# Optimization experiments

Measured on AMD Instinct MI355X. Metric: run time of the kernel, lower is better.

Reference implementation:

```python
import jax, jax.numpy as jnp
import numpy as np

N_RAYS = 4096
WORLD_LEN = 160
K0_DIM = 12
WIDTH = 128
VIEWPE = 4
BG_LEN = 0.2
XYZ_MIN = -1.0 - BG_LEN
XYZ_MAX = 1.0 + BG_LEN
ALPHA_INIT = 1e-4
ACT_SHIFT = float(np.log(1.0 / (1.0 - ALPHA_INIT) - 1.0))  # density bias shift
BG = 1.0  # background color (render_kwargs['bg'])
DIM0 = 3 + 3 * VIEWPE * 2 + K0_DIM  # 39


def grid_interp(grid, pts):
    """Trilinear interpolation (align_corners=True). grid: [C,R,R,R], pts: [M,3] world coords -> [M,C]."""
    R = grid.shape[1]
    g = (pts - XYZ_MIN) / (XYZ_MAX - XYZ_MIN) * (R - 1)
    g = jnp.clip(g, 0.0, R - 1)
    g0 = jnp.clip(jnp.floor(g).astype(jnp.int32), 0, R - 2)
    f = g - g0
    x0, y0, z0 = g0[:, 0], g0[:, 1], g0[:, 2]
    fx, fy, fz = f[:, 0], f[:, 1], f[:, 2]

    def gat(i, j, k):
        return grid[:, i, j, k]  # [C, M]

    c00 = gat(x0, y0, z0) * (1 - fz) + gat(x0, y0, z0 + 1) * fz
    c01 = gat(x0, y0 + 1, z0) * (1 - fz) + gat(x0, y0 + 1, z0 + 1) * fz
    c10 = gat(x0 + 1, y0, z0) * (1 - fz) + gat(x0 + 1, y0, z0 + 1) * fz
    c11 = gat(x0 + 1, y0 + 1, z0) * (1 - fz) + gat(x0 + 1, y0 + 1, z0 + 1) * fz
    c0 = c00 * (1 - fy) + c01 * fy
    c1 = c10 * (1 - fy) + c11 * fy
    return (c0 * (1 - fx) + c1 * fx).T  # [M, C]


def setup_inputs() -> dict:
    key = jax.random.key(0)
    ks = jax.random.split(key, 11)
    return {
        "rays_o": jax.random.normal(ks[0], (N_RAYS, 3), jnp.float32) * 0.3,
        "rays_d": jax.random.normal(ks[1], (N_RAYS, 3), jnp.float32),
        "viewdirs": jax.random.normal(ks[2], (N_RAYS, 3), jnp.float32),
        "density_grid": jax.random.normal(ks[3], (1, WORLD_LEN, WORLD_LEN, WORLD_LEN), jnp.float32),
        "k0_grid": jax.random.normal(ks[4], (K0_DIM, WORLD_LEN, WORLD_LEN, WORLD_LEN), jnp.float32),
        "w0": jax.random.normal(ks[5], (DIM0, WIDTH), jnp.float32) * 0.05,
        "b0": jnp.zeros((WIDTH,), jnp.float32),
        "w1": jax.random.normal(ks[6], (WIDTH, WIDTH), jnp.float32) * 0.05,
        "b1": jnp.zeros((WIDTH,), jnp.float32),
        "w2": jax.random.normal(ks[7], (WIDTH, 3), jnp.float32) * 0.05,
        "b2": jnp.zeros((3,), jnp.float32),
        "stepsize": 1,
    }


def reference(rays_o, rays_d, viewdirs, density_grid, k0_grid, w0, b0, w1, b1, w2, b2, stepsize):
    sqrt3 = float(np.sqrt(3.0))
    # --- sample_ray: sample points along rays in the contracted domain ---
    N_inner = int(2.0 / (2.0 + 2.0 * BG_LEN) * sqrt3 * WORLD_LEN / stepsize) + 1
    N_outer = int(N_inner * max(0.01, BG_LEN / 2.0))
    b_inner = jnp.linspace(0.0, 2.0 * sqrt3, N_inner + 1)
    b_outer = 2.0 * sqrt3 / jnp.linspace(1.0, 0.001, N_outer + 1)
    t = jnp.concatenate([(b_inner[1:] + b_inner[:-1]) * 0.5,
                         (b_outer[1:] + b_outer[:-1]) * 0.5])  # [P]
    # scene_center = 0, scene_radius = 1 for xyz_min=-1, xyz_max=1
    rd = rays_d / jnp.linalg.norm(rays_d, axis=-1, keepdims=True)
    pts = rays_o[:, None, :] + rd[:, None, :] * t[None, :, None]  # [N,P,3]
    norm = jnp.max(jnp.abs(pts), axis=-1, keepdims=True)
    safe = jnp.maximum(norm, 1e-9)
    pts = jnp.where(norm <= 1.0, pts, pts / safe * (1.0 + BG_LEN - BG_LEN / safe))
    N, P = pts.shape[0], pts.shape[1]
    flat = pts.reshape(-1, 3)  # [M,3]

    # --- density -> alpha (Raw2Alpha); mask_cache is all-True, fast_color_thres=0 ---
    interval = float(stepsize) * 1.0  # voxel_size_ratio == 1
    dens = grid_interp(density_grid, flat)[:, 0].reshape(N, P)
    alpha = 1.0 - jnp.power(1.0 + jnp.exp(dens + ACT_SHIFT), -interval)

    # --- Alphas2Weights: per-ray alpha compositing ---
    T = jnp.cumprod(1.0 - alpha, axis=1)
    T_excl = jnp.concatenate([jnp.ones((N, 1), T.dtype), T[:, :-1]], axis=1)
    weights = alpha * T_excl  # [N,P]
    alphainv_last = T[:, -1]  # [N]

    # --- k0 features + view-dependent MLP ---
    k0 = grid_interp(k0_grid, flat).reshape(N, P, K0_DIM)
    vf = (2.0 ** jnp.arange(VIEWPE)).astype(rays_o.dtype)
    ve = (viewdirs[..., None] * vf).reshape(N, -1)
    vemb = jnp.concatenate([viewdirs, jnp.sin(ve), jnp.cos(ve)], axis=-1)  # [N, 3+24]
    feat = jnp.concatenate(
        [k0, jnp.broadcast_to(vemb[:, None, :], (N, P, vemb.shape[-1]))], axis=-1)  # [N,P,39]
    h = jax.nn.relu(feat @ w0 + b0)
    h = jax.nn.relu(h @ w1 + b1)
    rgb = jax.nn.sigmoid(h @ w2 + b2)  # [N,P,3]

    # --- volume rendering ---
    rgb_marched = jnp.sum(weights[..., None] * rgb, axis=1) + alphainv_last[:, None] * BG
    return rgb_marched  # [N,3]
```

## Files before the change

### kernel.cpp

```cpp
#include <hip/hip_runtime.h>

#define NRAYS 4096
#define PSAMP 254
#define NIN   231
#define GR    160
#define GR2   25600
#define GR3   4096000
#define SROW  136

typedef __attribute__((ext_vector_type(8))) short bf16x8;
typedef __attribute__((ext_vector_type(4))) float f32x4;

__device__ __forceinline__ unsigned short f2bf(float x) {
    union { float f; unsigned u; } v; v.f = x;
    return (unsigned short)((v.u + 0x7fffu + ((v.u >> 16) & 1u)) >> 16);
}
__device__ __forceinline__ float sigmoidf_(float x) { return 1.0f / (1.0f + __expf(-x)); }

__device__ __forceinline__ unsigned packh2(float a, float b) {
    union { _Float16 h; unsigned short u; } ua, ub;
    ua.h = (_Float16)a; ub.h = (_Float16)b;
    return (unsigned)ua.u | ((unsigned)ub.u << 16);
}
__device__ __forceinline__ float h2f(unsigned u16) {
    union { unsigned short u; _Float16 h; } v; v.u = (unsigned short)u16;
    return (float)v.h;
}
__device__ __forceinline__ float cget(const uint4& q, int c) {
    const unsigned w = ((const unsigned*)&q)[c >> 1];
    return h2f((c & 1) ? (w >> 16) : (w & 0xffffu));
}

__global__ void prepack(const float* __restrict__ w, unsigned short* __restrict__ out,
                        int K, int N, int ldw, int NT, int KS) {
    const int idx = blockIdx.x * 256 + threadIdx.x;
    if (idx >= NT * KS * 64) return;
    const int l  = idx & 63, f = idx >> 6;
    const int ks = f % KS,  nt = f / KS;
    const int n  = nt * 16 + (l & 15);
    const int k0 = ks * 32 + (l >> 4) * 8;
    unsigned p[4];
    #pragma unroll
    for (int q = 0; q < 4; q++) {
        const int ka = k0 + 2 * q, kb = ka + 1;
        const float va = (ka < K && n < N) ? w[ka * ldw + n] : 0.0f;
        const float vb = (kb < K && n < N) ? w[kb * ldw + n] : 0.0f;
        p[q] = (unsigned)f2bf(va) | ((unsigned)f2bf(vb) << 16);
    }
    uint4 v; v.x = p[0]; v.y = p[1]; v.z = p[2]; v.w = p[3];
    ((uint4*)out)[idx] = v;
}

__global__ __launch_bounds__(256) void repack_grid(
    const float* __restrict__ dg, const float* __restrict__ k0g,
    unsigned short* __restrict__ pg)
{
    const int i2 = blockIdx.x * 256 + threadIdx.x;
    if (i2 >= GR3 / 2) return;
    unsigned ow[16];
    #pragma unroll
    for (int c = 0; c < 12; c += 2) {
        const float2 va = ((const float2*)(k0g + (size_t)c       * GR3))[i2];
        const float2 vb = ((const float2*)(k0g + (size_t)(c + 1) * GR3))[i2];
        ow[(c >> 1)]     = packh2(va.x, vb.x);
        ow[8 + (c >> 1)] = packh2(va.y, vb.y);
    }
    const float2 dv = ((const float2*)dg)[i2];
    ow[6]  = packh2(dv.x, 0.0f);
    ow[14] = packh2(dv.y, 0.0f);
    ow[7] = 0u; ow[15] = 0u;
    uint4* dst = (uint4*)(pg + (size_t)i2 * 32);
    dst[0] = make_uint4(ow[0],  ow[1],  ow[2],  ow[3]);
    dst[1] = make_uint4(ow[4],  ow[5],  ow[6],  ow[7]);
    dst[2] = make_uint4(ow[8],  ow[9],  ow[10], ow[11]);
    dst[3] = make_uint4(ow[12], ow[13], ow[14], ow[15]);
}

__global__ __launch_bounds__(256, 2) void voxgo_mfma_pk(
    const float* __restrict__ rays_o, const float* __restrict__ rays_d,
    const float* __restrict__ viewdirs,
    const unsigned short* __restrict__ pg,
    const float* __restrict__ b0, const float* __restrict__ b1,
    const float* __restrict__ b2,
    const unsigned short* __restrict__ pw0, const unsigned short* __restrict__ pw1,
    const unsigned short* __restrict__ pw2,
    float* __restrict__ out)
{
    const int r    = blockIdx.x;
    const int tid  = threadIdx.x;
    const int wv   = tid >> 6, lane = tid & 63, quad = lane >> 4, l16 = lane & 15;

    __shared__ unsigned short hbuf[4][64 * SROW];
    __shared__ float sc[256];
    __shared__ float wgt[256];
    __shared__ float redbuf[256];

    const float ox = rays_o[3*r+0], oy = rays_o[3*r+1], oz = rays_o[3*r+2];
    float dxv = rays_d[3*r+0], dyv = rays_d[3*r+1], dzv = rays_d[3*r+2];
    const float vdx = viewdirs[3*r+0], vdy = viewdirs[3*r+1], vdz = viewdirs[3*r+2];
    const float rinv = rsqrtf(dxv*dxv + dyv*dyv + dzv*dzv);
    dxv *= rinv; dyv *= rinv; dzv *= rinv;

    float t;
    if (tid < NIN) {
        t = ((float)tid + 0.5f) * (2.0f * 1.7320508075688772f / 231.0f);
    } else {
        const float lstep = 0.999f / 23.0f;
        const int j = tid - NIN;
        const float L0 = 1.0f - (float)j * lstep;
        const float L1 = 1.0f - (float)(j+1) * lstep;
        t = 1.7320508075688772f * (1.0f/L0 + 1.0f/L1);
    }

    float px = fmaf(dxv, t, ox), py = fmaf(dyv, t, oy), pz = fmaf(dzv, t, oz);
    const float nrm = fmaxf(fabsf(px), fmaxf(fabsf(py), fabsf(pz)));
    if (nrm > 1.0f) {
        const float s = (1.2f - 0.2f / nrm) / nrm;
        px *= s; py *= s; pz *= s;
    }

    const float gsc = 159.0f / 2.4f;
    const float gx = fminf(fmaxf((px + 1.2f) * gsc, 0.0f), 159.0f);
    const float gy = fminf(fmaxf((py + 1.2f) * gsc, 0.0f), 159.0f);
    const float gz = fminf(fmaxf((pz + 1.2f) * gsc, 0.0f), 159.0f);
    const int x0 = min((int)gx, GR-2), y0 = min((int)gy, GR-2), z0 = min((int)gz, GR-2);
    const float fx = gx - (float)x0, fy = gy - (float)y0, fz = gz - (float)z0;
    const int base = x0*GR2 + y0*GR + z0;

    const unsigned short* cp = pg + (size_t)base * 16;
    uint4 hi[8], lo[8];
    #pragma unroll
    for (int j = 0; j < 8; j++) {
        const int off = ((j >> 2) * GR2 + ((j >> 1) & 1) * GR + (j & 1)) * 16;
        hi[j] = *((const uint4*)(cp + off) + 1);
    }
    #pragma unroll
    for (int j = 0; j < 8; j++) {
        const int off = ((j >> 2) * GR2 + ((j >> 1) & 1) * GR + (j & 1)) * 16;
        lo[j] = *((const uint4*)(cp + off));
    }

    float fv[40];
    fv[12] = vdx; fv[13] = vdy; fv[14] = vdz;
    #pragma unroll
    for (int p = 0; p < 4; p++) {
        const float f = (float)(1 << p);
        fv[15+p] = __sinf(vdx*f);  fv[19+p] = __sinf(vdy*f);  fv[23+p] = __sinf(vdz*f);
        fv[27+p] = __cosf(vdx*f);  fv[31+p] = __cosf(vdy*f);  fv[35+p] = __cosf(vdz*f);
    }
    fv[39] = 0.0f;

    float dcr[8];
    #pragma unroll
    for (int j = 0; j < 8; j++) dcr[j] = h2f(hi[j].z & 0xffffu);
    const float c00 = dcr[0]*(1.0f-fz) + dcr[1]*fz;
    const float c01 = dcr[2]*(1.0f-fz) + dcr[3]*fz;
    const float c10 = dcr[4]*(1.0f-fz) + dcr[5]*fz;
    const float c11 = dcr[6]*(1.0f-fz) + dcr[7]*fz;
    const float dens = (c00*(1.0f-fy) + c01*fy)*(1.0f-fx) + (c10*(1.0f-fy) + c11*fy)*fx;

    const float ACT_SHIFT = -9.21024036697535f;
    const float alpha = (tid < PSAMP) ? sigmoidf_(dens + ACT_SHIFT) : 0.0f;

    sc[tid] = 1.0f - alpha;
    __syncthreads();
    #pragma unroll
    for (int off = 1; off < 256; off <<= 1) {
        const float v = (tid >= off) ? sc[tid - off] : 1.0f;
        __syncthreads();
        sc[tid] *= v;
        __syncthreads();
    }
    const float T_excl = (tid == 0) ? 1.0f : sc[tid-1];
    wgt[tid] = alpha * T_excl;

    const float wx0 = 1.0f-fx, wy0 = 1.0f-fy, wz0 = 1.0f-fz;
    const float w000 = wx0*wy0*wz0, w001 = wx0*wy0*fz, w010 = wx0*fy*wz0, w011 = wx0*fy*fz;
    const float w100 = fx*wy0*wz0,  w101 = fx*wy0*fz,  w110 = fx*fy*wz0,  w111 = fx*fy*fz;

    #pragma unroll
    for (int c = 0; c < 12; c++) {
        float s;
        if (c < 8) {
            s = w000*cget(lo[0],c) + w001*cget(lo[1],c)
              + w010*cget(lo[2],c) + w011*cget(lo[3],c)
              + w100*cget(lo[4],c) + w101*cget(lo[5],c)
              + w110*cget(lo[6],c) + w111*cget(lo[7],c);
        } else {
            s = w000*cget(hi[0],c-8) + w001*cget(hi[1],c-8)
              + w010*cget(hi[2],c-8) + w011*cget(hi[3],c-8)
              + w100*cget(hi[4],c-8) + w101*cget(hi[5],c-8)
              + w110*cget(hi[6],c-8) + w111*cget(hi[7],c-8);
        }
        fv[c] = s;
    }

    unsigned short* hb = &hbuf[wv][0];
    {
        const int row = tid & 63;
        uint4* dst = (uint4*)(hb + row * SROW);
        #pragma unroll
        for (int i = 0; i < 8; i++) {
            unsigned p[4];
            #pragma unroll
            for (int q = 0; q < 4; q++) {
                const int e0 = i*8 + 2*q, e1 = e0 + 1;
                const unsigned plo = (e0 < 39) ? f2bf(fv[e0]) : 0u;
                const unsigned phi = (e1 < 39) ? f2bf(fv[e1]) : 0u;
                p[q] = plo | (phi << 16);
            }
            uint4 v; v.x = p[0]; v.y = p[1]; v.z = p[2]; v.w = p[3];
            dst[i] = v;
        }
    }
    __syncthreads();

    f32x4 acc1[4][8];
    #pragma unroll
    for (int nt = 0; nt < 8; nt++) {
        const float bz = b0[nt*16 + l16];
        #pragma unroll
        for (int mt = 0; mt < 4; mt++) { f32x4 z = {bz,bz,bz,bz}; acc1[mt][nt] = z; }
    }
    #pragma unroll
    for (int ks = 0; ks < 2; ks++) {
        bf16x8 a[4];
        #pragma unroll
        for (int mt = 0; mt < 4; mt++)
            a[mt] = *(const bf16x8*)(hb + (mt*16 + l16)*SROW + ks*32 + quad*8);
        #pragma unroll
        for (int nt = 0; nt < 8; nt++) {
            const bf16x8 b = *(const bf16x8*)(pw0 + ((nt*2 + ks)*64 + lane)*8);
            #pragma unroll
            for (int mt = 0; mt < 4; mt++)
                acc1[mt][nt] = __builtin_amdgcn_mfma_f32_16x16x32_bf16(a[mt], b, acc1[mt][nt], 0,0,0);
        }
    }
    #pragma unroll
    for (int mt = 0; mt < 4; mt++)
        #pragma unroll
        for (int nt = 0; nt < 8; nt++)
            #pragma unroll
            for (int e = 0; e < 4; e++)
                hb[(mt*16 + quad*4 + e)*SROW + nt*16 + l16] = f2bf(fmaxf(acc1[mt][nt][e], 0.0f));
    __syncthreads();

    f32x4 acc2[4][8];
    #pragma unroll
    for (int nt = 0; nt < 8; nt++) {
        const float bz = b1[nt*16 + l16];
        #pragma unroll
        for (int mt = 0; mt < 4; mt++) { f32x4 z = {bz,bz,bz,bz}; acc2[mt][nt] = z; }
    }
    #pragma unroll
    for (int ks = 0; ks < 4; ks++) {
        bf16x8 a[4];
        #pragma unroll
        for (int mt = 0; mt < 4; mt++)
            a[mt] = *(const bf16x8*)(hb + (mt*16 + l16)*SROW + ks*32 + quad*8);
        #pragma unroll
        for (int nt = 0; nt < 8; nt++) {
            const bf16x8 b = *(const bf16x8*)(pw1 + ((nt*4 + ks)*64 + lane)*8);
            #pragma unroll
            for (int mt = 0; mt < 4; mt++)
                acc2[mt][nt] = __builtin_amdgcn_mfma_f32_16x16x32_bf16(a[mt], b, acc2[mt][nt], 0,0,0);
        }
    }
    #pragma unroll
    for (int mt = 0; mt < 4; mt++)
        #pragma unroll
        for (int nt = 0; nt < 8; nt++)
            #pragma unroll
            for (int e = 0; e < 4; e++)
                hb[(mt*16 + quad*4 + e)*SROW + nt*16 + l16] = f2bf(fmaxf(acc2[mt][nt][e], 0.0f));
    __syncthreads();

    f32x4 acc3[4];
    {
        const float bz = (l16 < 3) ? b2[l16] : 0.0f;
        #pragma unroll
        for (int mt = 0; mt < 4; mt++) { f32x4 z = {bz,bz,bz,bz}; acc3[mt] = z; }
    }
    #pragma unroll
    for (int ks = 0; ks < 4; ks++) {
        const bf16x8 b = *(const bf16x8*)(pw2 + (ks*64 + lane)*8);
        #pragma unroll
        for (int mt = 0; mt < 4; mt++) {
            const bf16x8 a = *(const bf16x8*)(hb + (mt*16 + l16)*SROW + ks*32 + quad*8);
            acc3[mt] = __builtin_amdgcn_mfma_f32_16x16x32_bf16(a, b, acc3[mt], 0,0,0);
        }
    }

    float contrib = 0.0f;
    #pragma unroll
    for (int mt = 0; mt < 4; mt++)
        #pragma unroll
        for (int e = 0; e < 4; e++) {
            const float s = sigmoidf_(acc3[mt][e]);
            contrib += wgt[wv*64 + mt*16 + quad*4 + e] * s;
        }
    redbuf[tid] = contrib;
    __syncthreads();
    if (tid < 3) {
        float acc_o = sc[PSAMP-1];
        #pragma unroll
        for (int w = 0; w < 4; w++)
            #pragma unroll
            for (int q = 0; q < 4; q++)
                acc_o += redbuf[w*64 + q*16 + tid];
        out[3*r + tid] = acc_o;
    }
}

__global__ __launch_bounds__(256, 2) void voxgo_mfma_f32(
    const float* __restrict__ rays_o, const float* __restrict__ rays_d,
    const float* __restrict__ viewdirs, const float* __restrict__ dg,
    const float* __restrict__ k0g,
    const float* __restrict__ b0, const float* __restrict__ b1,
    const float* __restrict__ b2,
    const unsigned short* __restrict__ pw0, const unsigned short* __restrict__ pw1,
    const unsigned short* __restrict__ pw2,
    float* __restrict__ out)
{
    const int r    = blockIdx.x;
    const int tid  = threadIdx.x;
    const int wv   = tid >> 6, lane = tid & 63, quad = lane >> 4, l16 = lane & 15;

    __shared__ unsigned short hbuf[4][64 * SROW];
    __shared__ float sc[256];
    __shared__ float wgt[256];
    __shared__ float redbuf[256];

    const float ox = rays_o[3*r+0], oy = rays_o[3*r+1], oz = rays_o[3*r+2];
    float dxv = rays_d[3*r+0], dyv = rays_d[3*r+1], dzv = rays_d[3*r+2];
    const float vdx = viewdirs[3*r+0], vdy = viewdirs[3*r+1], vdz = viewdirs[3*r+2];
    const float rinv = rsqrtf(dxv*dxv + dyv*dyv + dzv*dzv);
    dxv *= rinv; dyv *= rinv; dzv *= rinv;

    float t;
    if (tid < NIN) {
        t = ((float)tid + 0.5f) * (2.0f * 1.7320508075688772f / 231.0f);
    } else {
        const float lstep = 0.999f / 23.0f;
        const int j = tid - NIN;
        const float L0 = 1.0f - (float)j * lstep;
        const float L1 = 1.0f - (float)(j+1) * lstep;
        t = 1.7320508075688772f * (1.0f/L0 + 1.0f/L1);
    }

    float px = fmaf(dxv, t, ox), py = fmaf(dyv, t, oy), pz = fmaf(dzv, t, oz);
    const float nrm = fmaxf(fabsf(px), fmaxf(fabsf(py), fabsf(pz)));
    if (nrm > 1.0f) {
        const float s = (1.2f - 0.2f / nrm) / nrm;
        px *= s; py *= s; pz *= s;
    }

    const float gsc = 159.0f / 2.4f;
    const float gx = fminf(fmaxf((px + 1.2f) * gsc, 0.0f), 159.0f);
    const float gy = fminf(fmaxf((py + 1.2f) * gsc, 0.0f), 159.0f);
    const float gz = fminf(fmaxf((pz + 1.2f) * gsc, 0.0f), 159.0f);
    const int x0 = min((int)gx, GR-2), y0 = min((int)gy, GR-2), z0 = min((int)gz, GR-2);
    const float fx = gx - (float)x0, fy = gy - (float)y0, fz = gz - (float)z0;
    const int base = x0*GR2 + y0*GR + z0;

    const float d000 = dg[base],        d001 = dg[base+1];
    const float d010 = dg[base+GR],     d011 = dg[base+GR+1];
    const float d100 = dg[base+GR2],    d101 = dg[base+GR2+1];
    const float d110 = dg[base+GR2+GR], d111 = dg[base+GR2+GR+1];
    const float c00 = d000*(1.0f-fz) + d001*fz;
    const float c01 = d010*(1.0f-fz) + d011*fz;
    const float c10 = d100*(1.0f-fz) + d101*fz;
    const float c11 = d110*(1.0f-fz) + d111*fz;
    const float dens = (c00*(1.0f-fy) + c01*fy)*(1.0f-fx) + (c10*(1.0f-fy) + c11*fy)*fx;

    const float ACT_SHIFT = -9.21024036697535f;
    const float alpha = (tid < PSAMP) ? sigmoidf_(dens + ACT_SHIFT) : 0.0f;

    sc[tid] = 1.0f - alpha;
    __syncthreads();
    #pragma unroll
    for (int off = 1; off < 256; off <<= 1) {
        const float v = (tid >= off) ? sc[tid - off] : 1.0f;
        __syncthreads();
        sc[tid] *= v;
        __syncthreads();
    }
    const float T_excl = (tid == 0) ? 1.0f : sc[tid-1];
    wgt[tid] = alpha * T_excl;

    const float wx0 = 1.0f-fx, wy0 = 1.0f-fy, wz0 = 1.0f-fz;
    const float w000 = wx0*wy0*wz0, w001 = wx0*wy0*fz, w010 = wx0*fy*wz0, w011 = wx0*fy*fz;
    const float w100 = fx*wy0*wz0,  w101 = fx*wy0*fz,  w110 = fx*fy*wz0,  w111 = fx*fy*fz;

    float fv[40];
    #pragma unroll
    for (int c = 0; c < 12; c++) {
        const float* g = k0g + c*GR3 + base;
        fv[c] = w000*g[0]      + w001*g[1]
              + w010*g[GR]     + w011*g[GR+1]
              + w100*g[GR2]    + w101*g[GR2+1]
              + w110*g[GR2+GR] + w111*g[GR2+GR+1];
    }
    fv[12] = vdx; fv[13] = vdy; fv[14] = vdz;
    #pragma unroll
    for (int p = 0; p < 4; p++) {
        const float f = (float)(1 << p);
        fv[15+p] = __sinf(vdx*f);  fv[19+p] = __sinf(vdy*f);  fv[23+p] = __sinf(vdz*f);
        fv[27+p] = __cosf(vdx*f);  fv[31+p] = __cosf(vdy*f);  fv[35+p] = __cosf(vdz*f);
    }
    fv[39] = 0.0f;

    unsigned short* hb = &hbuf[wv][0];
    {
        const int row = tid & 63;
        uint4* dst = (uint4*)(hb + row * SROW);
        #pragma unroll
        for (int i = 0; i < 8; i++) {
            unsigned p[4];
            #pragma unroll
            for (int q = 0; q < 4; q++) {
                const int e0 = i*8 + 2*q, e1 = e0 + 1;
                const unsigned lov = (e0 < 39) ? f2bf(fv[e0]) : 0u;
                const unsigned hiv = (e1 < 39) ? f2bf(fv[e1]) : 0u;
                p[q] = lov | (hiv << 16);
            }
            uint4 v; v.x = p[0]; v.y = p[1]; v.z = p[2]; v.w = p[3];
            dst[i] = v;
        }
    }
    __syncthreads();

    f32x4 acc1[4][8];
    #pragma unroll
    for (int nt = 0; nt < 8; nt++) {
        const float bz = b0[nt*16 + l16];
        #pragma unroll
        for (int mt = 0; mt < 4; mt++) { f32x4 z = {bz,bz,bz,bz}; acc1[mt][nt] = z; }
    }
    #pragma unroll
    for (int ks = 0; ks < 2; ks++) {
        bf16x8 a[4];
        #pragma unroll
        for (int mt = 0; mt < 4; mt++)
            a[mt] = *(const bf16x8*)(hb + (mt*16 + l16)*SROW + ks*32 + quad*8);
        #pragma unroll
        for (int nt = 0; nt < 8; nt++) {
            const bf16x8 b = *(const bf16x8*)(pw0 + ((nt*2 + ks)*64 + lane)*8);
            #pragma unroll
            for (int mt = 0; mt < 4; mt++)
                acc1[mt][nt] = __builtin_amdgcn_mfma_f32_16x16x32_bf16(a[mt], b, acc1[mt][nt], 0,0,0);
        }
    }
    #pragma unroll
    for (int mt = 0; mt < 4; mt++)
        #pragma unroll
        for (int nt = 0; nt < 8; nt++)
            #pragma unroll
            for (int e = 0; e < 4; e++)
                hb[(mt*16 + quad*4 + e)*SROW + nt*16 + l16] = f2bf(fmaxf(acc1[mt][nt][e], 0.0f));
    __syncthreads();

    f32x4 acc2[4][8];
    #pragma unroll
    for (int nt = 0; nt < 8; nt++) {
        const float bz = b1[nt*16 + l16];
        #pragma unroll
        for (int mt = 0; mt < 4; mt++) { f32x4 z = {bz,bz,bz,bz}; acc2[mt][nt] = z; }
    }
    #pragma unroll
    for (int ks = 0; ks < 4; ks++) {
        bf16x8 a[4];
        #pragma unroll
        for (int mt = 0; mt < 4; mt++)
            a[mt] = *(const bf16x8*)(hb + (mt*16 + l16)*SROW + ks*32 + quad*8);
        #pragma unroll
        for (int nt = 0; nt < 8; nt++) {
            const bf16x8 b = *(const bf16x8*)(pw1 + ((nt*4 + ks)*64 + lane)*8);
            #pragma unroll
            for (int mt = 0; mt < 4; mt++)
                acc2[mt][nt] = __builtin_amdgcn_mfma_f32_16x16x32_bf16(a[mt], b, acc2[mt][nt], 0,0,0);
        }
    }
    #pragma unroll
    for (int mt = 0; mt < 4; mt++)
        #pragma unroll
        for (int nt = 0; nt < 8; nt++)
            #pragma unroll
            for (int e = 0; e < 4; e++)
                hb[(mt*16 + quad*4 + e)*SROW + nt*16 + l16] = f2bf(fmaxf(acc2[mt][nt][e], 0.0f));
    __syncthreads();

    f32x4 acc3[4];
    {
        const float bz = (l16 < 3) ? b2[l16] : 0.0f;
        #pragma unroll
        for (int mt = 0; mt < 4; mt++) { f32x4 z = {bz,bz,bz,bz}; acc3[mt] = z; }
    }
    #pragma unroll
    for (int ks = 0; ks < 4; ks++) {
        const bf16x8 b = *(const bf16x8*)(pw2 + (ks*64 + lane)*8);
        #pragma unroll
        for (int mt = 0; mt < 4; mt++) {
            const bf16x8 a = *(const bf16x8*)(hb + (mt*16 + l16)*SROW + ks*32 + quad*8);
            acc3[mt] = __builtin_amdgcn_mfma_f32_16x16x32_bf16(a, b, acc3[mt], 0,0,0);
        }
    }

    float contrib = 0.0f;
    #pragma unroll
    for (int mt = 0; mt < 4; mt++)
        #pragma unroll
        for (int e = 0; e < 4; e++) {
            const float s = sigmoidf_(acc3[mt][e]);
            contrib += wgt[wv*64 + mt*16 + quad*4 + e] * s;
        }
    redbuf[tid] = contrib;
    __syncthreads();
    if (tid < 3) {
        float acc_o = sc[PSAMP-1];
        #pragma unroll
        for (int w = 0; w < 4; w++)
            #pragma unroll
            for (int q = 0; q < 4; q++)
                acc_o += redbuf[w*64 + q*16 + tid];
        out[3*r + tid] = acc_o;
    }
}

extern "C" void kernel_launch(void* const* d_in, const int* in_sizes, int n_in,
                              void* d_out, int out_size, void* d_ws, size_t ws_size,
                              hipStream_t stream) {
    (void)in_sizes; (void)n_in; (void)out_size;
    const size_t PG_BYTES = (size_t)GR3 * 32;
    const size_t PW_BYTES = (size_t)(16 + 32 + 4) * 64 * 8 * 2;

    if (ws_size >= PG_BYTES + PW_BYTES) {
        unsigned short* pg  = (unsigned short*)d_ws;
        unsigned short* pw0 = (unsigned short*)((char*)d_ws + PG_BYTES);
        unsigned short* pw1 = pw0 + 16*64*8;
        unsigned short* pw2 = pw1 + 32*64*8;

        repack_grid<<<GR3/512, 256, 0, stream>>>(
            (const float*)d_in[3], (const float*)d_in[4], pg);
        prepack<<<4, 256, 0, stream>>>((const float*)d_in[5], pw0,  39, 128, 128, 8, 2);
        prepack<<<8, 256, 0, stream>>>((const float*)d_in[7], pw1, 128, 128, 128, 8, 4);
        prepack<<<1, 256, 0, stream>>>((const float*)d_in[9], pw2, 128,   3,   3, 1, 4);

        voxgo_mfma_pk<<<NRAYS, 256, 0, stream>>>(
            (const float*)d_in[0], (const float*)d_in[1], (const float*)d_in[2],
            pg,
            (const float*)d_in[6], (const float*)d_in[8], (const float*)d_in[10],
            pw0, pw1, pw2,
            (float*)d_out);
    } else {
        unsigned short* pw0 = (unsigned short*)d_ws;
        unsigned short* pw1 = pw0 + 16*64*8;
        unsigned short* pw2 = pw1 + 32*64*8;

        prepack<<<4, 256, 0, stream>>>((const float*)d_in[5], pw0,  39, 128, 128, 8, 2);
        prepack<<<8, 256, 0, stream>>>((const float*)d_in[7], pw1, 128, 128, 128, 8, 4);
        prepack<<<1, 256, 0, stream>>>((const float*)d_in[9], pw2, 128,   3,   3, 1, 4);

        voxgo_mfma_f32<<<NRAYS, 256, 0, stream>>>(
            (const float*)d_in[0], (const float*)d_in[1], (const float*)d_in[2],
            (const float*)d_in[3], (const float*)d_in[4],
            (const float*)d_in[6], (const float*)d_in[8], (const float*)d_in[10],
            pw0, pw1, pw2,
            (float*)d_out);
    }
}
```

Baseline: 457.4 us.

## Use wave-shuffle scan, transposed MFMA layout, packed bf16 converts, fewer block barriers

Result: faster. 438.4 us (-4.1%).

```diff
diff --git a/kernel.cpp b/kernel.cpp
--- a/kernel.cpp
+++ b/kernel.cpp
@@ -16,6 +16,12 @@
     return (unsigned short)((v.u + 0x7fffu + ((v.u >> 16) & 1u)) >> 16);
 }
 __device__ __forceinline__ float sigmoidf_(float x) { return 1.0f / (1.0f + __expf(-x)); }
+
+__device__ __forceinline__ unsigned cvt_pk_bf16(float a, float b) {
+    unsigned r;
+    asm("v_cvt_pk_bf16_f32 %0, %1, %2" : "=v"(r) : "v"(a), "v"(b));
+    return r;
+}
 
 __device__ __forceinline__ unsigned packh2(float a, float b) {
     union { _Float16 h; unsigned short u; } ua, ub;
@@ -91,9 +97,9 @@
     const int wv   = tid >> 6, lane = tid & 63, quad = lane >> 4, l16 = lane & 15;
 
     __shared__ unsigned short hbuf[4][64 * SROW];
-    __shared__ float sc[256];
     __shared__ float wgt[256];
-    __shared__ float redbuf[256];
+    __shared__ float redbuf[4 * 16 * 3];
+    __shared__ float wtot[4];
 
     const float ox = rays_o[3*r+0], oy = rays_o[3*r+1], oz = rays_o[3*r+2];
     float dxv = rays_d[3*r+0], dyv = rays_d[3*r+1], dzv = rays_d[3*r+2];
@@ -162,16 +168,19 @@
     const float ACT_SHIFT = -9.21024036697535f;
     const float alpha = (tid < PSAMP) ? sigmoidf_(dens + ACT_SHIFT) : 0.0f;
 
-    sc[tid] = 1.0f - alpha;
-    __syncthreads();
-    #pragma unroll
-    for (int off = 1; off < 256; off <<= 1) {
-        const float v = (tid >= off) ? sc[tid - off] : 1.0f;
-        __syncthreads();
-        sc[tid] *= v;
-        __syncthreads();
-    }
-    const float T_excl = (tid == 0) ? 1.0f : sc[tid-1];
+    float vscan = 1.0f - alpha;
+    #pragma unroll
+    for (int off = 1; off < 64; off <<= 1) {
+        const float u = __shfl_up(vscan, off);
+        if (lane >= off) vscan *= u;
+    }
+    if (lane == 63) wtot[wv] = vscan;
+    __syncthreads();
+    float pre = 1.0f;
+    #pragma unroll
+    for (int w = 0; w < 3; w++) if (w < wv) pre *= wtot[w];
+    const float eprev = __shfl_up(vscan, 1);
+    const float T_excl = (lane == 0) ? pre : pre * eprev;
     wgt[tid] = alpha * T_excl;
 
     const float wx0 = 1.0f-fx, wy0 = 1.0f-fy, wz0 = 1.0f-fz;
@@ -205,109 +214,113 @@
             #pragma unroll
             for (int q = 0; q < 4; q++) {
                 const int e0 = i*8 + 2*q, e1 = e0 + 1;
-                const unsigned plo = (e0 < 39) ? f2bf(fv[e0]) : 0u;
-                const unsigned phi = (e1 < 39) ? f2bf(fv[e1]) : 0u;
-                p[q] = plo | (phi << 16);
+                const float a = (e0 < 39) ? fv[e0] : 0.0f;
+                const float b = (e1 < 39) ? fv[e1] : 0.0f;
+                p[q] = cvt_pk_bf16(a, b);
             }
             uint4 v; v.x = p[0]; v.y = p[1]; v.z = p[2]; v.w = p[3];
             dst[i] = v;
         }
     }
-    __syncthreads();
-
-    f32x4 acc1[4][8];
-    #pragma unroll
-    for (int nt = 0; nt < 8; nt++) {
-        const float bz = b0[nt*16 + l16];
-        #pragma unroll
-        for (int mt = 0; mt < 4; mt++) { f32x4 z = {bz,bz,bz,bz}; acc1[mt][nt] = z; }
+
+
+    f32x4 acc1[8][4];
+    #pragma unroll
+    for (int ft = 0; ft < 8; ft++) {
+        const f32x4 bv = *(const f32x4*)(b0 + ft*16 + quad*4);
+        #pragma unroll
+        for (int st = 0; st < 4; st++) acc1[ft][st] = bv;
     }
     #pragma unroll
     for (int ks = 0; ks < 2; ks++) {
-        bf16x8 a[4];
-        #pragma unroll
-        for (int mt = 0; mt < 4; mt++)
-            a[mt] = *(const bf16x8*)(hb + (mt*16 + l16)*SROW + ks*32 + quad*8);
-        #pragma unroll
-        for (int nt = 0; nt < 8; nt++) {
-            const bf16x8 b = *(const bf16x8*)(pw0 + ((nt*2 + ks)*64 + lane)*8);
-            #pragma unroll
-            for (int mt = 0; mt < 4; mt++)
-                acc1[mt][nt] = __builtin_amdgcn_mfma_f32_16x16x32_bf16(a[mt], b, acc1[mt][nt], 0,0,0);
-        }
-    }
-    #pragma unroll
-    for (int mt = 0; mt < 4; mt++)
-        #pragma unroll
-        for (int nt = 0; nt < 8; nt++)
-            #pragma unroll
-            for (int e = 0; e < 4; e++)
-                hb[(mt*16 + quad*4 + e)*SROW + nt*16 + l16] = f2bf(fmaxf(acc1[mt][nt][e], 0.0f));
-    __syncthreads();
-
-    f32x4 acc2[4][8];
-    #pragma unroll
-    for (int nt = 0; nt < 8; nt++) {
-        const float bz = b1[nt*16 + l16];
-        #pragma unroll
-        for (int mt = 0; mt < 4; mt++) { f32x4 z = {bz,bz,bz,bz}; acc2[mt][nt] = z; }
+        bf16x8 bfr[4];
+        #pragma unroll
+        for (int st = 0; st < 4; st++)
+            bfr[st] = *(const bf16x8*)(hb + (st*16 + l16)*SROW + ks*32 + quad*8);
+        #pragma unroll
+        for (int ft = 0; ft < 8; ft++) {
+            const bf16x8 afr = *(const bf16x8*)(pw0 + ((ft*2 + ks)*64 + lane)*8);
+            #pragma unroll
+            for (int st = 0; st < 4; st++)
+                acc1[ft][st] = __builtin_amdgcn_mfma_f32_16x16x32_bf16(afr, bfr[st], acc1[ft][st], 0,0,0);
+        }
+    }
+    #pragma unroll
+    for (int ft = 0; ft < 8; ft++)
+        #pragma unroll
+        for (int st = 0; st < 4; st++) {
+            const f32x4 a = acc1[ft][st];
+            uint2 v;
+            v.x = cvt_pk_bf16(fmaxf(a[0], 0.0f), fmaxf(a[1], 0.0f));
+            v.y = cvt_pk_bf16(fmaxf(a[2], 0.0f), fmaxf(a[3], 0.0f));
+            *(uint2*)(hb + (st*16 + l16)*SROW + ft*16 + quad*4) = v;
+        }
+
+    f32x4 acc2[8][4];
+    #pragma unroll
+    for (int ft = 0; ft < 8; ft++) {
+        const f32x4 bv = *(const f32x4*)(b1 + ft*16 + quad*4);
+        #pragma unroll
+        for (int st = 0; st < 4; st++) acc2[ft][st] = bv;
     }
     #pragma unroll
     for (int ks = 0; ks < 4; ks++) {
-        bf16x8 a[4];
-        #pragma unroll
-        for (int mt = 0; mt < 4; mt++)
-            a[mt] = *(const bf16x8*)(hb + (mt*16 + l16)*SROW + ks*32 + quad*8);
-        #pragma unroll
-        for (int nt = 0; nt < 8; nt++) {
-            const bf16x8 b = *(const bf16x8*)(pw1 + ((nt*4 + ks)*64 + lane)*8);
-            #pragma unroll
-            for (int mt = 0; mt < 4; mt++)
-                acc2[mt][nt] = __builtin_amdgcn_mfma_f32_16x16x32_bf16(a[mt], b, acc2[mt][nt], 0,0,0);
-        }
-    }
-    #pragma unroll
-    for (int mt = 0; mt < 4; mt++)
-        #pragma unroll
-        for (int nt = 0; nt < 8; nt++)
-            #pragma unroll
-            for (int e = 0; e < 4; e++)
-                hb[(mt*16 + quad*4 + e)*SROW + nt*16 + l16] = f2bf(fmaxf(acc2[mt][nt][e], 0.0f));
-    __syncthreads();
+        bf16x8 bfr[4];
+        #pragma unroll
+        for (int st = 0; st < 4; st++)
+            bfr[st] = *(const bf16x8*)(hb + (st*16 + l16)*SROW + ks*32 + quad*8);
+        #pragma unroll
+        for (int ft = 0; ft < 8; ft++) {
+            const bf16x8 afr = *(const bf16x8*)(pw1 + ((ft*4 + ks)*64 + lane)*8);
+            #pragma unroll
+            for (int st = 0; st < 4; st++)
+                acc2[ft][st] = __builtin_amdgcn_mfma_f32_16x16x32_bf16(afr, bfr[st], acc2[ft][st], 0,0,0);
+        }
+    }
+    #pragma unroll
+    for (int ft = 0; ft < 8; ft++)
+        #pragma unroll
+        for (int st = 0; st < 4; st++) {
+            const f32x4 a = acc2[ft][st];
+            uint2 v;
+            v.x = cvt_pk_bf16(fmaxf(a[0], 0.0f), fmaxf(a[1], 0.0f));
+            v.y = cvt_pk_bf16(fmaxf(a[2], 0.0f), fmaxf(a[3], 0.0f));
+            *(uint2*)(hb + (st*16 + l16)*SROW + ft*16 + quad*4) = v;
+        }
 
     f32x4 acc3[4];
     {
-        const float bz = (l16 < 3) ? b2[l16] : 0.0f;
-        #pragma unroll
-        for (int mt = 0; mt < 4; mt++) { f32x4 z = {bz,bz,bz,bz}; acc3[mt] = z; }
+        f32x4 bz3; bz3[0] = b2[0]; bz3[1] = b2[1]; bz3[2] = b2[2]; bz3[3] = 0.0f;
+        #pragma unroll
+        for (int st = 0; st < 4; st++) acc3[st] = bz3;
     }
     #pragma unroll
     for (int ks = 0; ks < 4; ks++) {
-        const bf16x8 b = *(const bf16x8*)(pw2 + (ks*64 + lane)*8);
-        #pragma unroll
-        for (int mt = 0; mt < 4; mt++) {
-            const bf16x8 a = *(const bf16x8*)(hb + (mt*16 + l16)*SROW + ks*32 + quad*8);
-            acc3[mt] = __builtin_amdgcn_mfma_f32_16x16x32_bf16(a, b, acc3[mt], 0,0,0);
-        }
-    }
-
-    float contrib = 0.0f;
-    #pragma unroll
-    for (int mt = 0; mt < 4; mt++)
-        #pragma unroll
-        for (int e = 0; e < 4; e++) {
-            const float s = sigmoidf_(acc3[mt][e]);
-            contrib += wgt[wv*64 + mt*16 + quad*4 + e] * s;
-        }
-    redbuf[tid] = contrib;
+        const bf16x8 afr = *(const bf16x8*)(pw2 + (ks*64 + lane)*8);
+        #pragma unroll
+        for (int st = 0; st < 4; st++) {
+            const bf16x8 bfr = *(const bf16x8*)(hb + (st*16 + l16)*SROW + ks*32 + quad*8);
+            acc3[st] = __builtin_amdgcn_mfma_f32_16x16x32_bf16(afr, bfr, acc3[st], 0,0,0);
+        }
+    }
+
+    if (quad == 0) {
+        float c0 = 0.0f, c1 = 0.0f, c2 = 0.0f;
+        #pragma unroll
+        for (int st = 0; st < 4; st++) {
+            const float w = wgt[wv*64 + st*16 + l16];
+            c0 += w * sigmoidf_(acc3[st][0]);
+            c1 += w * sigmoidf_(acc3[st][1]);
+            c2 += w * sigmoidf_(acc3[st][2]);
+        }
+        float* rb = &redbuf[(wv*16 + l16)*3];
+        rb[0] = c0; rb[1] = c1; rb[2] = c2;
+    }
     __syncthreads();
     if (tid < 3) {
-        float acc_o = sc[PSAMP-1];
-        #pragma unroll
-        for (int w = 0; w < 4; w++)
-            #pragma unroll
-            for (int q = 0; q < 4; q++)
-                acc_o += redbuf[w*64 + q*16 + tid];
+        float acc_o = wtot[0]*wtot[1]*wtot[2]*wtot[3];
+        #pragma unroll 4
+        for (int i = 0; i < 64; i++) acc_o += redbuf[i*3 + tid];
         out[3*r + tid] = acc_o;
     }
 }
```
